# Kernel optimization log

Hardware: AMD Instinct MI355X
Metric: run time of the kernel (lower is better)

The kernel has to match this reference:

```python
import jax, jax.numpy as jnp
import numpy as np

N_NODES = 100000
N_EDGES = 1250000
IN_NDIM = 128
OUT_NDIM = 64


def setup_inputs() -> dict:
    key = jax.random.key(0)
    ks = jax.random.split(key, 8)
    return {
        "node_feats": jax.random.normal(ks[0], (N_NODES, IN_NDIM), dtype=jnp.float32),
        "edge_d": jax.random.uniform(ks[1], (N_EDGES, 1), dtype=jnp.float32),
        "W0": jax.random.normal(ks[2], (1, 1), dtype=jnp.float32),
        "W1": jax.random.normal(ks[3], (OUT_NDIM, IN_NDIM), dtype=jnp.float32) * (IN_NDIM ** -0.5),
        "W2": jax.random.normal(ks[4], (OUT_NDIM, IN_NDIM), dtype=jnp.float32) * (IN_NDIM ** -0.5),
        "Wa": jax.random.normal(ks[5], (1, 2 * OUT_NDIM + 1), dtype=jnp.float32) * (OUT_NDIM ** -0.5),
        "src": jax.random.randint(ks[6], (N_EDGES,), 0, N_NODES, dtype=jnp.int32),
        "dst": jax.random.randint(ks[7], (N_EDGES,), 0, N_NODES, dtype=jnp.int32),
    }


def reference(node_feats, edge_d, W0, W1, W2, Wa, src, dst):
    N = node_feats.shape[0]
    # fc1 / fc2 node projections (bias-free linears)
    z = node_feats @ W1.T            # [N, out_ndim]
    z_i = node_feats @ W2.T          # [N, out_ndim]
    # fc0 edge feature projection
    t = edge_d @ W0.T                # [E, 1]
    # gather per-edge endpoint features
    z_src = z[src]                   # [E, out_ndim]
    z_dst = z[dst]                   # [E, out_ndim]
    # attention logit: leaky_relu(attn_fc([z_src, z_dst, t]))
    a = jnp.concatenate([z_src, z_dst, t], axis=1) @ Wa.T   # [E, 1]
    e = jax.nn.leaky_relu(a[:, 0], 0.01)                      # torch default slope
    # segment softmax over incoming edges of each dst node
    m = jax.ops.segment_max(e, dst, num_segments=N)          # -inf for empty segs
    ex = jnp.exp(e - m[dst])
    denom = jax.ops.segment_sum(ex, dst, num_segments=N)
    alpha = ex / denom[dst]                                   # [E]
    # weighted scatter-sum of source messages
    z_neighbor = jax.ops.segment_sum(alpha[:, None] * z_src, dst, num_segments=N)
    h = jax.nn.relu(z_i + z_neighbor)
    return h
```

## Files before the change

kernel.cpp:

```cpp
#include <hip/hip_runtime.h>

#define N_NODES 100000
#define N_EDGES 1250000
#define IN_D 128
#define OUT_D 64
#define BSHIFT 7
#define NBUCK  782
#define CAP    2560
#define EPB    4096
#define NBLK_E 306
#define NBLK_G 1563

typedef __attribute__((ext_vector_type(8))) __bf16 bf16x8;
typedef __attribute__((ext_vector_type(4))) float floatx4;

__device__ __forceinline__ float2 up2(unsigned u) {
    return make_float2(__uint_as_float(u << 16),
                       __uint_as_float(u & 0xFFFF0000u));
}

__global__ __launch_bounds__(256) void fusedA_kernel(
    const float* __restrict__ x, const float* __restrict__ W1,
    const float* __restrict__ W2, const float* __restrict__ W0,
    const float* __restrict__ Wa,
    const int* __restrict__ dst, const int* __restrict__ src,
    const float* __restrict__ edge_d,
    int* __restrict__ gcur, uint2* __restrict__ payA,
    unsigned short* __restrict__ zb, unsigned short* __restrict__ zib,
    float* __restrict__ s1, float* __restrict__ s2)
{
    __shared__ __bf16 sB[16384];
    __shared__ float  sWa[128];
    __shared__ int    h[NBUCK];
    __shared__ int    lcur[NBUCK];

    const int t = threadIdx.x;

    if (blockIdx.x < NBLK_E) {
        const float tc = W0[0] * Wa[2 * OUT_D];
        for (int i = t; i < NBUCK; i += 256) h[i] = 0;
        __syncthreads();
        const int base = blockIdx.x * EPB;
        int4 d4[4], rk4[4]; bool val[4];
        #pragma unroll
        for (int k = 0; k < 4; ++k) {
            int i = base + k * 1024 + t * 4;
            val[k] = (i < N_EDGES);
            if (val[k]) {
                d4[k] = *(const int4*)(dst + i);
                rk4[k].x = atomicAdd(&h[d4[k].x >> BSHIFT], 1);
                rk4[k].y = atomicAdd(&h[d4[k].y >> BSHIFT], 1);
                rk4[k].z = atomicAdd(&h[d4[k].z >> BSHIFT], 1);
                rk4[k].w = atomicAdd(&h[d4[k].w >> BSHIFT], 1);
            }
        }
        __syncthreads();
        for (int b = t; b < NBUCK; b += 256) {
            int hc = h[b];
            int p = hc ? atomicAdd(&gcur[b], hc) : 0;
            lcur[b] = b * CAP + p;
        }
        __syncthreads();
        #define EMIT(dv, sv, ev, rk)                                          \
            { int bk = (dv) >> BSHIFT;                                        \
              int pos = lcur[bk] + (rk);                                      \
              if (pos < (bk + 1) * CAP)                                       \
                  payA[pos] = make_uint2((unsigned)(sv) |                     \
                                         ((unsigned)((dv) & 127) << 17),      \
                                         __float_as_uint(tc * (ev))); }
        #pragma unroll
        for (int k = 0; k < 4; ++k) {
            int i = base + k * 1024 + t * 4;
            if (val[k]) {
                int4   s4 = *(const int4*)(src + i);
                float4 e4 = *(const float4*)(edge_d + i);
                EMIT(d4[k].x, s4.x, e4.x, rk4[k].x);
                EMIT(d4[k].y, s4.y, e4.y, rk4[k].y);
                EMIT(d4[k].z, s4.z, e4.z, rk4[k].z);
                EMIT(d4[k].w, s4.w, e4.w, rk4[k].w);
            }
        }
        #undef EMIT
        return;
    }

    #pragma unroll
    for (int g = 0; g < 8; ++g) {
        int gi = t + g * 256;
        int n  = gi >> 4;
        int k8 = gi & 15;
        const float* wrow = (n < 64) ? (W1 + n * 128) : (W2 + (n - 64) * 128);
        float4 v0 = *(const float4*)(wrow + k8 * 8);
        float4 v1 = *(const float4*)(wrow + k8 * 8 + 4);
        int lane = ((k8 & 3) << 4) | (n & 15);
        int off  = (((n >> 4) * 4 + (k8 >> 2)) * 64 + lane) * 8;
        bf16x8 bb;
        bb[0] = (__bf16)v0.x; bb[1] = (__bf16)v0.y;
        bb[2] = (__bf16)v0.z; bb[3] = (__bf16)v0.w;
        bb[4] = (__bf16)v1.x; bb[5] = (__bf16)v1.y;
        bb[6] = (__bf16)v1.z; bb[7] = (__bf16)v1.w;
        *(bf16x8*)(sB + off) = bb;
    }
    if (t < 128) sWa[t] = Wa[t];
    __syncthreads();

    const int lane = t & 63;
    const int wave = t >> 6;
    const int tile = (blockIdx.x - NBLK_E) * 4 + wave;
    if (tile * 16 >= N_NODES) return;

    const int n0 = tile * 16;
    const int m  = lane & 15;
    const int kb = lane >> 4;

    floatx4 acc[8];
    #pragma unroll
    for (int q = 0; q < 8; ++q) acc[q] = (floatx4)(0.f);

    const float* xrow = x + (size_t)(n0 + m) * IN_D;

    #pragma unroll
    for (int kc = 0; kc < 4; ++kc) {
        float4 v0 = *(const float4*)(xrow + kc * 32 + kb * 8);
        float4 v1 = *(const float4*)(xrow + kc * 32 + kb * 8 + 4);
        float xs[8] = {v0.x, v0.y, v0.z, v0.w, v1.x, v1.y, v1.z, v1.w};
        bf16x8 ahi, alo;
        #pragma unroll
        for (int j = 0; j < 8; ++j) {
            __bf16 hh = (__bf16)xs[j];
            ahi[j] = hh;
            alo[j] = (__bf16)(xs[j] - (float)hh);
        }
        #pragma unroll
        for (int nt = 0; nt < 8; ++nt) {
            int off = ((nt * 4 + kc) * 64 + lane) * 8;
            bf16x8 b = *(const bf16x8*)(sB + off);
            acc[nt] = __builtin_amdgcn_mfma_f32_16x16x32_bf16(ahi, b, acc[nt], 0, 0, 0);
            acc[nt] = __builtin_amdgcn_mfma_f32_16x16x32_bf16(alo, b, acc[nt], 0, 0, 0);
        }
    }

    #pragma unroll
    for (int nt = 0; nt < 8; ++nt) {
        int col = (nt & 3) * 16 + m;
        unsigned short* dp = (nt < 4) ? zb : zib;
        #pragma unroll
        for (int reg = 0; reg < 4; ++reg) {
            int row = n0 + kb * 4 + reg;
            __bf16 hh = (__bf16)acc[nt][reg];
            dp[(size_t)row * OUT_D + col] = *(unsigned short*)&hh;
        }
    }

    #pragma unroll
    for (int reg = 0; reg < 4; ++reg) {
        float p1 = 0.f, p2 = 0.f;
        #pragma unroll
        for (int nt = 0; nt < 4; ++nt) {
            float zv = acc[nt][reg];
            p1 += zv * sWa[nt * 16 + m];
            p2 += zv * sWa[64 + nt * 16 + m];
        }
        #pragma unroll
        for (int off = 8; off > 0; off >>= 1) {
            p1 += __shfl_xor(p1, off);
            p2 += __shfl_xor(p2, off);
        }
        if (m == 0) {
            int row = n0 + kb * 4 + reg;
            s1[row] = p1;
            s2[row] = p2;
        }
    }
}

__global__ __launch_bounds__(512) void sortgather_kernel(
    const int* __restrict__ gcur, const uint2* __restrict__ payA,
    const float* __restrict__ s1, const float* __restrict__ s2,
    const unsigned short* __restrict__ zb, const unsigned short* __restrict__ zib,
    float* __restrict__ out)
{
    __shared__ uint2 sorted[CAP];
    __shared__ int   h[128];
    __shared__ int   st[128];
    __shared__ int   lc[128];
    __shared__ float s2s[128];
    __shared__ uint2 buf[16][32];

    const int b = blockIdx.x, t = threadIdx.x;
    const int n0 = b << BSHIFT;
    const int base = b * CAP;
    const int cnt = min(gcur[b], CAP);
    const int lane = t & 63;
    const int wave = t >> 6;

    if (t < 128) {
        h[t] = 0;
        int node = n0 + t;
        s2s[t] = (node < N_NODES) ? s2[node] : 0.f;
    }
    __syncthreads();

    for (int i = t; i < cnt; i += 512) {
        uint2 p = payA[base + i];
        atomicAdd(&h[(p.x >> 17) & 127], 1);
    }
    __syncthreads();

    if (wave == 0) {
        int v0 = h[lane];
        int v1 = h[lane + 64];
        int s0 = v0, s1v = v1;
        #pragma unroll
        for (int off = 1; off < 64; off <<= 1) {
            int u0 = __shfl_up(s0, off);
            int u1 = __shfl_up(s1v, off);
            if (lane >= off) { s0 += u0; s1v += u1; }
        }
        int tot0 = __shfl(s0, 63);
        s1v += tot0;
        int e0 = s0 - v0, e1 = s1v - v1;
        st[lane] = e0;      lc[lane] = e0;
        st[lane + 64] = e1; lc[lane + 64] = e1;
    }
    __syncthreads();

    for (int i = t; i < cnt; i += 512) {
        uint2 p = payA[base + i];
        int dl = (p.x >> 17) & 127;
        int pos = atomicAdd(&lc[dl], 1);
        sorted[pos] = make_uint2(p.x & 0x1FFFFu, p.y);
    }
    __syncthreads();

    const int half = lane >> 5;
    const int lh   = lane & 31;
    const int slot = wave * 2 + half;
    const int eC = lh >> 3;
    const int c  = lh & 7;

    for (int r = 0; r < 8; ++r) {
        const int ln   = slot + r * 16;
        const int node = n0 + ln;
        const int beg  = st[ln];
        const int len  = h[ln];
        const float s2d = s2s[ln];

        float den = 0.f;
        float2 a0 = make_float2(0.f, 0.f), a1 = a0, a2 = a0, a3 = a0;

        for (int o = 0; o < len; o += 32) {
            int rem = len - o;
            bool vv = lh < rem;
            uint2 p = sorted[beg + o + (vv ? lh : 0)];
            float ex = 0.f;
            if (vv) {
                float a = __uint_as_float(p.y) + s1[p.x] + s2d;
                float e = (a > 0.f) ? a : 0.01f * a;
                ex = __expf(e);
                buf[slot][lh] = make_uint2(p.x, __float_as_uint(ex));
            }
            den += ex;

            int cnt2 = min(32, rem);
            int nIt = (cnt2 + 3) >> 2;
            uint2 pe = buf[slot][(eC < cnt2) ? eC : 0];
            float exe = (eC < cnt2) ? __uint_as_float(pe.y) : 0.f;
            uint4 zv = *(const uint4*)(zb + (size_t)pe.x * OUT_D + c * 8);
            for (int g = 0; g < nIt; ++g) {
                uint2 peN; float exeN = 0.f; uint4 zvN;
                if (g + 1 < nIt) {
                    int j = (g + 1) * 4 + eC;
                    peN  = buf[slot][(j < cnt2) ? j : 0];
                    exeN = (j < cnt2) ? __uint_as_float(peN.y) : 0.f;
                    zvN  = *(const uint4*)(zb + (size_t)peN.x * OUT_D + c * 8);
                }
                float2 w0 = up2(zv.x), w1 = up2(zv.y), w2 = up2(zv.z), w3 = up2(zv.w);
                a0.x = fmaf(exe, w0.x, a0.x); a0.y = fmaf(exe, w0.y, a0.y);
                a1.x = fmaf(exe, w1.x, a1.x); a1.y = fmaf(exe, w1.y, a1.y);
                a2.x = fmaf(exe, w2.x, a2.x); a2.y = fmaf(exe, w2.y, a2.y);
                a3.x = fmaf(exe, w3.x, a3.x); a3.y = fmaf(exe, w3.y, a3.y);
                pe = peN; exe = exeN; zv = zvN;
            }
        }

        #pragma unroll
        for (int off = 16; off > 0; off >>= 1) den += __shfl_xor(den, off);
        #pragma unroll
        for (int off = 8; off <= 16; off <<= 1) {
            a0.x += __shfl_xor(a0.x, off); a0.y += __shfl_xor(a0.y, off);
            a1.x += __shfl_xor(a1.x, off); a1.y += __shfl_xor(a1.y, off);
            a2.x += __shfl_xor(a2.x, off); a2.y += __shfl_xor(a2.y, off);
            a3.x += __shfl_xor(a3.x, off); a3.y += __shfl_xor(a3.y, off);
        }

        if (lh < 8 && node < N_NODES) {
            float inv = (den > 0.f) ? 1.f / den : 0.f;
            uint4 zv = *(const uint4*)(zib + (size_t)node * OUT_D + lh * 8);
            float2 w0 = up2(zv.x), w1 = up2(zv.y), w2 = up2(zv.z), w3 = up2(zv.w);
            float4 o0, o1;
            o0.x = fmaxf(w0.x + a0.x * inv, 0.f);
            o0.y = fmaxf(w0.y + a0.y * inv, 0.f);
            o0.z = fmaxf(w1.x + a1.x * inv, 0.f);
            o0.w = fmaxf(w1.y + a1.y * inv, 0.f);
            o1.x = fmaxf(w2.x + a2.x * inv, 0.f);
            o1.y = fmaxf(w2.y + a2.y * inv, 0.f);
            o1.z = fmaxf(w3.x + a3.x * inv, 0.f);
            o1.w = fmaxf(w3.y + a3.y * inv, 0.f);
            *(float4*)(out + (size_t)node * OUT_D + lh * 8)     = o0;
            *(float4*)(out + (size_t)node * OUT_D + lh * 8 + 4) = o1;
        }
    }
}

extern "C" void kernel_launch(void* const* d_in, const int* in_sizes, int n_in,
                              void* d_out, int out_size, void* d_ws, size_t ws_size,
                              hipStream_t stream) {
    const float* node_feats = (const float*)d_in[0];
    const float* edge_d     = (const float*)d_in[1];
    const float* W0         = (const float*)d_in[2];
    const float* W1         = (const float*)d_in[3];
    const float* W2         = (const float*)d_in[4];
    const float* Wa         = (const float*)d_in[5];
    const int*   src        = (const int*)d_in[6];
    const int*   dst        = (const int*)d_in[7];
    float* out = (float*)d_out;

    char* ws = (char*)d_ws;
    uint2* payA = (uint2*)ws;    ws += (size_t)NBUCK * CAP * 8;
    unsigned short* zbuf = (unsigned short*)ws; ws += (size_t)N_NODES * OUT_D * 2;
    unsigned short* zib  = (unsigned short*)ws; ws += (size_t)N_NODES * OUT_D * 2;
    float* s1 = (float*)ws;      ws += (size_t)N_NODES * 4;
    float* s2 = (float*)ws;      ws += (size_t)N_NODES * 4;
    int*   gcur = (int*)ws;      ws += ((NBUCK + 3) & ~3) * 4;

    hipMemsetAsync(gcur, 0, NBUCK * 4, stream);

    fusedA_kernel<<<NBLK_E + NBLK_G, 256, 0, stream>>>(
        node_feats, W1, W2, W0, Wa, dst, src, edge_d,
        gcur, payA, zbuf, zib, s1, s2);

    sortgather_kernel<<<NBUCK, 512, 0, stream>>>(
        gcur, payA, s1, s2, zbuf, zib, out);
}
```

Measured before the change: 185.4 us.

## Stage GEMM outputs in LDS for coalesced 16-byte stores, use 512-thread blocks

The fused kernel moves to 512-thread blocks. Each GEMM block now handles 128 nodes across 8 waves and shares one bf16 copy of the weights between them, so the weights are converted half as often per node. The z/z_i results are staged through a padded LDS tile and written back as full 16-byte row segments rather than scattered 2-byte stores. The partition, weight and staging buffers share one LDS union to keep shared memory small. The cost is extra block-wide barriers, and the partition blocks now hold fewer edges per thread.

```diff
diff --git a/kernel.cpp b/kernel.cpp
--- a/kernel.cpp
+++ b/kernel.cpp
@@ -9,7 +9,9 @@
 #define CAP    2560
 #define EPB    4096
 #define NBLK_E 306
-#define NBLK_G 1563
+#define NTILE  6250
+#define NBLK_W 782
+#define SROW   72
 
 typedef __attribute__((ext_vector_type(8))) __bf16 bf16x8;
 typedef __attribute__((ext_vector_type(4))) float floatx4;
@@ -19,7 +21,7 @@
                        __uint_as_float(u & 0xFFFF0000u));
 }
 
-__global__ __launch_bounds__(256) void fusedA_kernel(
+__global__ __launch_bounds__(512, 8) void fusedA_kernel(
     const float* __restrict__ x, const float* __restrict__ W1,
     const float* __restrict__ W2, const float* __restrict__ W0,
     const float* __restrict__ Wa,
@@ -29,22 +31,26 @@
     unsigned short* __restrict__ zb, unsigned short* __restrict__ zib,
     float* __restrict__ s1, float* __restrict__ s2)
 {
-    __shared__ __bf16 sB[16384];
-    __shared__ float  sWa[128];
-    __shared__ int    h[NBUCK];
-    __shared__ int    lcur[NBUCK];
+    __shared__ union U {
+        struct { int h[NBUCK]; int lcur[NBUCK]; } pa;
+        struct { alignas(16) __bf16 sB[16384]; } ge;
+        struct { alignas(16) unsigned short st[2][128][SROW]; } cs;
+    } sm;
+    __shared__ float sWa[128];
 
     const int t = threadIdx.x;
 
     if (blockIdx.x < NBLK_E) {
+        int* h    = sm.pa.h;
+        int* lcur = sm.pa.lcur;
         const float tc = W0[0] * Wa[2 * OUT_D];
-        for (int i = t; i < NBUCK; i += 256) h[i] = 0;
+        for (int i = t; i < NBUCK; i += 512) h[i] = 0;
         __syncthreads();
         const int base = blockIdx.x * EPB;
-        int4 d4[4], rk4[4]; bool val[4];
-        #pragma unroll
-        for (int k = 0; k < 4; ++k) {
-            int i = base + k * 1024 + t * 4;
+        int4 d4[2], rk4[2]; bool val[2];
+        #pragma unroll
+        for (int k = 0; k < 2; ++k) {
+            int i = base + k * 2048 + t * 4;
             val[k] = (i < N_EDGES);
             if (val[k]) {
                 d4[k] = *(const int4*)(dst + i);
@@ -55,7 +61,7 @@
             }
         }
         __syncthreads();
-        for (int b = t; b < NBUCK; b += 256) {
+        for (int b = t; b < NBUCK; b += 512) {
             int hc = h[b];
             int p = hc ? atomicAdd(&gcur[b], hc) : 0;
             lcur[b] = b * CAP + p;
@@ -69,8 +75,8 @@
                                          ((unsigned)((dv) & 127) << 17),      \
                                          __float_as_uint(tc * (ev))); }
         #pragma unroll
-        for (int k = 0; k < 4; ++k) {
-            int i = base + k * 1024 + t * 4;
+        for (int k = 0; k < 2; ++k) {
+            int i = base + k * 2048 + t * 4;
             if (val[k]) {
                 int4   s4 = *(const int4*)(src + i);
                 float4 e4 = *(const float4*)(edge_d + i);
@@ -84,16 +90,17 @@
         return;
     }
 
+    __bf16* sB = sm.ge.sB;
     #pragma unroll
-    for (int g = 0; g < 8; ++g) {
-        int gi = t + g * 256;
+    for (int g = 0; g < 4; ++g) {
+        int gi = t + g * 512;
         int n  = gi >> 4;
         int k8 = gi & 15;
         const float* wrow = (n < 64) ? (W1 + n * 128) : (W2 + (n - 64) * 128);
         float4 v0 = *(const float4*)(wrow + k8 * 8);
         float4 v1 = *(const float4*)(wrow + k8 * 8 + 4);
-        int lane = ((k8 & 3) << 4) | (n & 15);
-        int off  = (((n >> 4) * 4 + (k8 >> 2)) * 64 + lane) * 8;
+        int ln  = ((k8 & 3) << 4) | (n & 15);
+        int off = (((n >> 4) * 4 + (k8 >> 2)) * 64 + ln) * 8;
         bf16x8 bb;
         bb[0] = (__bf16)v0.x; bb[1] = (__bf16)v0.y;
         bb[2] = (__bf16)v0.z; bb[3] = (__bf16)v0.w;
@@ -106,8 +113,9 @@
 
     const int lane = t & 63;
     const int wave = t >> 6;
-    const int tile = (blockIdx.x - NBLK_E) * 4 + wave;
-    if (tile * 16 >= N_NODES) return;
+    const int gb   = blockIdx.x - NBLK_E;
+    const int tile = gb * 8 + wave;
+    const bool valid = (tile < NTILE);
 
     const int n0 = tile * 16;
     const int m  = lane & 15;
@@ -117,59 +125,83 @@
     #pragma unroll
     for (int q = 0; q < 8; ++q) acc[q] = (floatx4)(0.f);
 
-    const float* xrow = x + (size_t)(n0 + m) * IN_D;
-
-    #pragma unroll
-    for (int kc = 0; kc < 4; ++kc) {
-        float4 v0 = *(const float4*)(xrow + kc * 32 + kb * 8);
-        float4 v1 = *(const float4*)(xrow + kc * 32 + kb * 8 + 4);
-        float xs[8] = {v0.x, v0.y, v0.z, v0.w, v1.x, v1.y, v1.z, v1.w};
-        bf16x8 ahi, alo;
-        #pragma unroll
-        for (int j = 0; j < 8; ++j) {
-            __bf16 hh = (__bf16)xs[j];
-            ahi[j] = hh;
-            alo[j] = (__bf16)(xs[j] - (float)hh);
-        }
+    if (valid) {
+        const float* xrow = x + (size_t)(n0 + m) * IN_D;
+        #pragma unroll
+        for (int kc = 0; kc < 4; ++kc) {
+            float4 v0 = *(const float4*)(xrow + kc * 32 + kb * 8);
+            float4 v1 = *(const float4*)(xrow + kc * 32 + kb * 8 + 4);
+            float xs[8] = {v0.x, v0.y, v0.z, v0.w, v1.x, v1.y, v1.z, v1.w};
+            bf16x8 ahi, alo;
+            #pragma unroll
+            for (int j = 0; j < 8; ++j) {
+                __bf16 hh = (__bf16)xs[j];
+                ahi[j] = hh;
+                alo[j] = (__bf16)(xs[j] - (float)hh);
+            }
+            #pragma unroll
+            for (int nt = 0; nt < 8; ++nt) {
+                int off = ((nt * 4 + kc) * 64 + lane) * 8;
+                bf16x8 b = *(const bf16x8*)(sB + off);
+                acc[nt] = __builtin_amdgcn_mfma_f32_16x16x32_bf16(ahi, b, acc[nt], 0, 0, 0);
+                acc[nt] = __builtin_amdgcn_mfma_f32_16x16x32_bf16(alo, b, acc[nt], 0, 0, 0);
+            }
+        }
+
+        #pragma unroll
+        for (int reg = 0; reg < 4; ++reg) {
+            float p1 = 0.f, p2 = 0.f;
+            #pragma unroll
+            for (int nt = 0; nt < 4; ++nt) {
+                float zv = acc[nt][reg];
+                p1 += zv * sWa[nt * 16 + m];
+                p2 += zv * sWa[64 + nt * 16 + m];
+            }
+            #pragma unroll
+            for (int off = 8; off > 0; off >>= 1) {
+                p1 += __shfl_xor(p1, off);
+                p2 += __shfl_xor(p2, off);
+            }
+            if (m == 0) {
+                int row = n0 + kb * 4 + reg;
+                s1[row] = p1;
+                s2[row] = p2;
+            }
+        }
+    }
+
+    __syncthreads();
+
+    if (valid) {
         #pragma unroll
         for (int nt = 0; nt < 8; ++nt) {
-            int off = ((nt * 4 + kc) * 64 + lane) * 8;
-            bf16x8 b = *(const bf16x8*)(sB + off);
-            acc[nt] = __builtin_amdgcn_mfma_f32_16x16x32_bf16(ahi, b, acc[nt], 0, 0, 0);
-            acc[nt] = __builtin_amdgcn_mfma_f32_16x16x32_bf16(alo, b, acc[nt], 0, 0, 0);
-        }
-    }
-
-    #pragma unroll
-    for (int nt = 0; nt < 8; ++nt) {
-        int col = (nt & 3) * 16 + m;
-        unsigned short* dp = (nt < 4) ? zb : zib;
-        #pragma unroll
-        for (int reg = 0; reg < 4; ++reg) {
-            int row = n0 + kb * 4 + reg;
-            __bf16 hh = (__bf16)acc[nt][reg];
-            dp[(size_t)row * OUT_D + col] = *(unsigned short*)&hh;
-        }
-    }
-
-    #pragma unroll
-    for (int reg = 0; reg < 4; ++reg) {
-        float p1 = 0.f, p2 = 0.f;
-        #pragma unroll
-        for (int nt = 0; nt < 4; ++nt) {
-            float zv = acc[nt][reg];
-            p1 += zv * sWa[nt * 16 + m];
-            p2 += zv * sWa[64 + nt * 16 + m];
-        }
-        #pragma unroll
-        for (int off = 8; off > 0; off >>= 1) {
-            p1 += __shfl_xor(p1, off);
-            p2 += __shfl_xor(p2, off);
-        }
-        if (m == 0) {
-            int row = n0 + kb * 4 + reg;
-            s1[row] = p1;
-            s2[row] = p2;
+            int mp  = nt >> 2;
+            int col = (nt & 3) * 16 + m;
+            #pragma unroll
+            for (int reg = 0; reg < 4; ++reg) {
+                int row = wave * 16 + kb * 4 + reg;
+                __bf16 hh = (__bf16)acc[nt][reg];
+                sm.cs.st[mp][row][col] = *(unsigned short*)&hh;
+            }
+        }
+    }
+    __syncthreads();
+
+    {
+        const int r  = t >> 2;
+        const int cb = (t & 3) * 16;
+        const int grow = gb * 128 + r;
+        if (grow < N_NODES) {
+            uint4 a0 = *(const uint4*)&sm.cs.st[0][r][cb];
+            uint4 a1 = *(const uint4*)&sm.cs.st[0][r][cb + 8];
+            uint4 b0 = *(const uint4*)&sm.cs.st[1][r][cb];
+            uint4 b1 = *(const uint4*)&sm.cs.st[1][r][cb + 8];
+            unsigned short* zp  = zb  + (size_t)grow * OUT_D + cb;
+            unsigned short* zip = zib + (size_t)grow * OUT_D + cb;
+            *(uint4*)zp        = a0;
+            *(uint4*)(zp + 8)  = a1;
+            *(uint4*)zip       = b0;
+            *(uint4*)(zip + 8) = b1;
         }
     }
 }
@@ -336,7 +368,7 @@
 
     hipMemsetAsync(gcur, 0, NBUCK * 4, stream);
 
-    fusedA_kernel<<<NBLK_E + NBLK_G, 256, 0, stream>>>(
+    fusedA_kernel<<<NBLK_E + NBLK_W, 512, 0, stream>>>(
         node_feats, W1, W2, W0, Wa, dst, src, edge_d,
         gcur, payA, zbuf, zib, s1, s2);
 
```

New measurement: 185.9 us. About the same (+0.3%).
